# Optimization experiments

Hardware: AMD Instinct MI355X
Metric: run time of the kernel (lower is better)

## Reference

```python
import jax, jax.numpy as jnp
import numpy as np

B, S, D, H = 1, 2048, 1280, 16
HD = D // H  # 80


def setup_inputs() -> dict:
    key = jax.random.key(0)
    ks = jax.random.split(key, 6)
    return {
        "hidden_states": jax.random.normal(ks[0], (B, S, D), dtype=jnp.float32),
        "rotary_pos_emb": jax.random.normal(ks[1], (S, HD // 2), dtype=jnp.float32),
        "qkv_w": jax.random.normal(ks[2], (3 * D, D), dtype=jnp.float32) * 0.02,
        "qkv_b": jax.random.normal(ks[3], (3 * D,), dtype=jnp.float32) * 0.02,
        "proj_w": jax.random.normal(ks[4], (D, D), dtype=jnp.float32) * 0.02,
        "proj_b": jax.random.normal(ks[5], (D,), dtype=jnp.float32) * 0.02,
    }


def reference(hidden_states, rotary_pos_emb, qkv_w, qkv_b, proj_w, proj_b):
    b, s, d = hidden_states.shape
    h = H
    hd = d // h
    scaling = hd ** -0.5

    # fused QKV projection: [b, s, 3*d]
    qkv = hidden_states @ qkv_w.T + qkv_b
    qkv = qkv.reshape(b, s, 3, h, hd)
    q, k, v = qkv[:, :, 0], qkv[:, :, 1], qkv[:, :, 2]  # each [b, s, h, hd]

    # rotary embedding: cos/sin [s, hd//2] -> [1, s, 1, hd]
    cos = jnp.cos(rotary_pos_emb)
    sin = jnp.sin(rotary_pos_emb)
    cos = jnp.concatenate([cos, cos], axis=-1)[None, :, None, :]
    sin = jnp.concatenate([sin, sin], axis=-1)[None, :, None, :]

    def apply_rope(x):
        x1, x2 = x[..., : hd // 2], x[..., hd // 2:]
        return x * cos + jnp.concatenate([-x2, x1], axis=-1) * sin

    q = apply_rope(q)
    k = apply_rope(k)

    # [b, h, s, hd]
    q = q.transpose(0, 2, 1, 3)
    k = k.transpose(0, 2, 1, 3)
    v = v.transpose(0, 2, 1, 3)

    # naive full attention matrix [b, h, s, s]
    attn = jnp.einsum("bhqd,bhkd->bhqk", q, k) * scaling
    attn = jax.nn.softmax(attn, axis=-1)
    out = jnp.einsum("bhqk,bhkd->bhqd", attn, v)
    out = out.transpose(0, 2, 1, 3).reshape(b, s, d)
    return out @ proj_w.T + proj_b
```

## Files before the change

kernel.cpp:

```cpp
#include <hip/hip_runtime.h>
#include <math.h>

#define SS 2048
#define DD 1280
#define HH 16
#define HDD 80
#define ND3 3840
#define ZZ 2

typedef __attribute__((ext_vector_type(8))) short short8;
typedef __attribute__((ext_vector_type(4))) short s16x4;
typedef __attribute__((ext_vector_type(4))) float f32x4;
typedef __attribute__((ext_vector_type(8))) _Float16 h16x8;
typedef __attribute__((ext_vector_type(4))) _Float16 h16x4;

__device__ inline short f2bf(float f) {
    union { float f; unsigned u; } x; x.f = f;
    unsigned r = x.u + 0x7FFF + ((x.u >> 16) & 1);
    return (short)(r >> 16);
}

__device__ inline void gload_lds16(const void* g, void* l) {
    __builtin_amdgcn_global_load_lds(
        (const __attribute__((address_space(1))) void*)g,
        (__attribute__((address_space(3))) void*)l, 16, 0, 0);
}

__global__ __launch_bounds__(256) void split_f16(
    const float* __restrict__ a, _Float16* __restrict__ ah, int nbA,
    const float* __restrict__ b, _Float16* __restrict__ bh, int nbB,
    const float* __restrict__ c, _Float16* __restrict__ ch)
{
    const float* x; _Float16* h;
    int blk = blockIdx.x;
    if (blk < nbA)            { x = a; h = ah; }
    else if (blk < nbA + nbB) { blk -= nbA; x = b; h = bh; }
    else                      { blk -= nbA + nbB; x = c; h = ch; }
    int i = (blk * 256 + threadIdx.x) * 4;
    float4 v = *(const float4*)(x + i);
    h16x4 hv;
    hv[0] = (_Float16)v.x; hv[1] = (_Float16)v.y;
    hv[2] = (_Float16)v.z; hv[3] = (_Float16)v.w;
    *(h16x4*)(h + i) = hv;
}

#define LDSA(m, kg) ((m) * 32 + (((kg) ^ (((m) >> 1) & 3)) << 3))

template <int BMT, int BNT>
__global__ __launch_bounds__(256) void gemm_f16(
    const _Float16* __restrict__ Ah, const _Float16* __restrict__ Bh,
    const float* __restrict__ bias, float* __restrict__ C,
    int M, int N, int K)
{
    constexpr int IT = BMT / 32;
    constexpr int JT = BNT / 32;
    constexpr int AU = BMT / 64;
    constexpr int BU = BNT / 64;
    __shared__ _Float16 AhS[BMT * 32];
    __shared__ _Float16 BhS[BNT * 32];

    const int tid = threadIdx.x;
    const int w = tid >> 6;
    const int lane = tid & 63;
    const int l15 = lane & 15;
    const int quad = lane >> 4;
    const int wm = w >> 1, wn = w & 1;
    const int bm = blockIdx.y * BMT;
    const int bn = blockIdx.x * BNT;

    f32x4 acc[IT][JT];
    #pragma unroll
    for (int i = 0; i < IT; ++i)
        #pragma unroll
        for (int j = 0; j < JT; ++j)
            acc[i][j] = (f32x4){0.f, 0.f, 0.f, 0.f};

    for (int k0 = 0; k0 < K; k0 += 32) {
        __syncthreads();
        #pragma unroll
        for (int u = 0; u < AU; ++u) {
            int i = tid + u * 256;
            int m = i >> 2;
            int kg = (i & 3) ^ ((m >> 1) & 3);
            gload_lds16(Ah + (size_t)(bm + m) * K + k0 + kg * 8,
                        &AhS[(i & ~63) * 8]);
        }
        #pragma unroll
        for (int u = 0; u < BU; ++u) {
            int i = tid + u * 256;
            int m = i >> 2;
            int kg = (i & 3) ^ ((m >> 1) & 3);
            gload_lds16(Bh + (size_t)(bn + m) * K + k0 + kg * 8,
                        &BhS[(i & ~63) * 8]);
        }
        __syncthreads();

        h16x8 af[IT], bf[JT];
        #pragma unroll
        for (int i = 0; i < IT; ++i) {
            int m = wm * (BMT / 2) + i * 16 + l15;
            af[i] = *(h16x8*)&AhS[LDSA(m, quad)];
        }
        #pragma unroll
        for (int j = 0; j < JT; ++j) {
            int n = wn * (BNT / 2) + j * 16 + l15;
            bf[j] = *(h16x8*)&BhS[LDSA(n, quad)];
        }
        #pragma unroll
        for (int i = 0; i < IT; ++i)
            #pragma unroll
            for (int j = 0; j < JT; ++j)
                acc[i][j] = __builtin_amdgcn_mfma_f32_16x16x32_f16(af[i], bf[j], acc[i][j], 0, 0, 0);
    }

    #pragma unroll
    for (int j = 0; j < JT; ++j) {
        int col = bn + wn * (BNT / 2) + j * 16 + l15;
        float bb = bias[col];
        #pragma unroll
        for (int i = 0; i < IT; ++i)
            #pragma unroll
            for (int r = 0; r < 4; ++r) {
                int row = bm + wm * (BMT / 2) + i * 16 + quad * 4 + r;
                C[(size_t)row * N + col] = acc[i][j][r] + bb;
            }
    }
}

__global__ __launch_bounds__(256) void gemm_proj_merge(
    const _Float16* __restrict__ o_part, const float* __restrict__ l_part,
    const _Float16* __restrict__ Bh,
    const float* __restrict__ bias, float* __restrict__ C,
    int M, int N, int K)
{
    constexpr int BMT = 64, BNT = 128;
    constexpr int JT = BNT / 32;
    constexpr int BU = BNT / 64;
    __shared__ _Float16 AhS[BMT * 32];
    __shared__ _Float16 BhS[BNT * 32];
    __shared__ float linvS[HH * 64];

    const int tid = threadIdx.x;
    const int w = tid >> 6;
    const int lane = tid & 63;
    const int l15 = lane & 15;
    const int quad = lane >> 4;
    const int wm = w >> 1, wn = w & 1;
    const int bm = blockIdx.y * BMT;
    const int bn = blockIdx.x * BNT;

    for (int i = tid; i < HH * 64; i += 256) {
        int h = i >> 6, r = i & 63;
        float ls = 0.f;
        #pragma unroll
        for (int zi = 0; zi < ZZ; ++zi)
            ls += l_part[((size_t)zi * HH + h) * SS + bm + r];
        linvS[i] = 1.f / ls;
    }

    f32x4 acc[2][JT];
    #pragma unroll
    for (int i = 0; i < 2; ++i)
        #pragma unroll
        for (int j = 0; j < JT; ++j)
            acc[i][j] = (f32x4){0.f, 0.f, 0.f, 0.f};

    h16x8 ra[ZZ];
    auto loadgA = [&](int k0) {
        int m = tid >> 2, kg = tid & 3;
        size_t off = (size_t)(bm + m) * K + k0 + kg * 8;
        #pragma unroll
        for (int zi = 0; zi < ZZ; ++zi)
            ra[zi] = *(const h16x8*)(o_part + (size_t)zi * SS * DD + off);
    };

    loadgA(0);
    for (int k0 = 0; k0 < K; k0 += 32) {
        __syncthreads();
        {
            int m = tid >> 2, kg = tid & 3;
            int koff = k0 + kg * 8;
            int h = koff / HDD;
            float inv = linvS[h * 64 + m];
            h16x8 f;
            #pragma unroll
            for (int e = 0; e < 8; ++e) {
                float s = (float)ra[0][e];
                #pragma unroll
                for (int zi = 1; zi < ZZ; ++zi) s += (float)ra[zi][e];
                f[e] = (_Float16)(s * inv);
            }
            *(h16x8*)&AhS[LDSA(m, kg)] = f;
        }
        #pragma unroll
        for (int u = 0; u < BU; ++u) {
            int i = tid + u * 256;
            int m = i >> 2;
            int kg = (i & 3) ^ ((m >> 1) & 3);
            gload_lds16(Bh + (size_t)(bn + m) * K + k0 + kg * 8,
                        &BhS[(i & ~63) * 8]);
        }
        __syncthreads();
        if (k0 + 32 < K) loadgA(k0 + 32);

        h16x8 af[2], bf[JT];
        #pragma unroll
        for (int i = 0; i < 2; ++i) {
            int m = wm * 32 + i * 16 + l15;
            af[i] = *(h16x8*)&AhS[LDSA(m, quad)];
        }
        #pragma unroll
        for (int j = 0; j < JT; ++j) {
            int n = wn * 64 + j * 16 + l15;
            bf[j] = *(h16x8*)&BhS[LDSA(n, quad)];
        }
        #pragma unroll
        for (int i = 0; i < 2; ++i)
            #pragma unroll
            for (int j = 0; j < JT; ++j)
                acc[i][j] = __builtin_amdgcn_mfma_f32_16x16x32_f16(af[i], bf[j], acc[i][j], 0, 0, 0);
    }

    #pragma unroll
    for (int j = 0; j < JT; ++j) {
        int col = bn + wn * 64 + j * 16 + l15;
        float bb = bias[col];
        #pragma unroll
        for (int i = 0; i < 2; ++i)
            #pragma unroll
            for (int r = 0; r < 4; ++r) {
                int row = bm + wm * 32 + i * 16 + quad * 4 + r;
                C[(size_t)row * N + col] = acc[i][j][r] + bb;
            }
    }
}

__global__ __launch_bounds__(256) void rope_scatter_bf16(
    const float* __restrict__ qkv, const float* __restrict__ rpe,
    short* __restrict__ q, short* __restrict__ k, short* __restrict__ v)
{
    __shared__ __align__(16) float cs[40], sn[40];
    const int s = blockIdx.x;
    if (threadIdx.x < 40)
        __sincosf(rpe[s * 40 + threadIdx.x], &sn[threadIdx.x], &cs[threadIdx.x]);
    __syncthreads();
    const float scale = 0.11180339887498949f;
    const float* src = qkv + (size_t)s * ND3;
    for (int t = threadIdx.x; t < ND3 / 4; t += 256) {
        int j4 = t * 4;
        int p = j4 / DD;
        int rem = j4 - p * DD;
        int hh = rem / HDD;
        int d = rem - hh * HDD;
        float4 x = *(const float4*)(src + j4);
        float vv[4];
        if (p == 2) {
            vv[0] = x.x; vv[1] = x.y; vv[2] = x.z; vv[3] = x.w;
        } else {
            bool lo = d < 40;
            int dm = lo ? d : d - 40;
            float4 oth = *(const float4*)(src + p * DD + hh * HDD + (lo ? d + 40 : d - 40));
            float4 c4 = *(const float4*)&cs[dm];
            float4 s4 = *(const float4*)&sn[dm];
            float sg = lo ? -1.f : 1.f;
            vv[0] = x.x * c4.x + sg * oth.x * s4.x;
            vv[1] = x.y * c4.y + sg * oth.y * s4.y;
            vv[2] = x.z * c4.z + sg * oth.z * s4.z;
            vv[3] = x.w * c4.w + sg * oth.w * s4.w;
            if (p == 0) { vv[0] *= scale; vv[1] *= scale; vv[2] *= scale; vv[3] *= scale; }
        }
        short* dst = (p == 0) ? q : (p == 1) ? k : v;
        s16x4 o4;
        o4[0] = f2bf(vv[0]); o4[1] = f2bf(vv[1]);
        o4[2] = f2bf(vv[2]); o4[3] = f2bf(vv[3]);
        *(s16x4*)(dst + ((size_t)hh * SS + s) * HDD + d) = o4;
    }
}

__global__ __launch_bounds__(512, 4) void attn_mfma(
    const short* __restrict__ q, const short* __restrict__ k,
    const short* __restrict__ v, _Float16* __restrict__ o_part,
    float* __restrict__ l_part)
{
    __shared__ short Ks[64][104];
    __shared__ short Vts[80 * 64];
    __shared__ short Ps[8][16 * 64];

    const int h = blockIdx.y;
    const int q0 = blockIdx.x << 7;
    const int z = blockIdx.z;
    const int tid = threadIdx.x;
    const int w = tid >> 6;
    const int lane = tid & 63;
    const int l15 = lane & 15;
    const int quad = lane >> 4;

    const short* qbase = q + (size_t)h * SS * HDD;
    const short* kbase = k + (size_t)h * SS * HDD;
    const short* vbase = v + (size_t)h * SS * HDD;

    short8 qf[3];
    {
        const int row = q0 + w * 16 + l15;
        #pragma unroll
        for (int kk = 0; kk < 3; ++kk) {
            int c0 = kk * 32 + quad * 8;
            qf[kk] = (c0 < HDD) ? *(const short8*)(qbase + (size_t)row * HDD + c0)
                                : (short8)0;
        }
    }

    if (tid < 128) {
        int r = tid >> 1, c = 80 + (tid & 1) * 8;
        *(short8*)&Ks[r][c] = (short8)0;
    }

    float lsum[4] = {0.f, 0.f, 0.f, 0.f};
    f32x4 o[5];
    #pragma unroll
    for (int n = 0; n < 5; ++n) o[n] = (f32x4){0.f, 0.f, 0.f, 0.f};

    const int kt0 = z << 10;
    for (int kt = kt0; kt < kt0 + 1024; kt += 64) {
        __syncthreads();
        #pragma unroll
        for (int u = 0; u < 2; ++u) {
            int i = tid + u * 512;
            if (i < 640) {
                int r = i / 10, c = (i - r * 10) * 8;
                *(short8*)&Ks[r][c] = *(const short8*)(kbase + (size_t)(kt + r) * HDD + c);
            }
        }
        {
            int task = tid;
            if (task < 320) {
                int r4 = (task & 15) << 2;
                int d4 = (task >> 4) << 2;
                s16x4 a0 = *(const s16x4*)(vbase + (size_t)(kt + r4 + 0) * HDD + d4);
                s16x4 a1 = *(const s16x4*)(vbase + (size_t)(kt + r4 + 1) * HDD + d4);
                s16x4 a2 = *(const s16x4*)(vbase + (size_t)(kt + r4 + 2) * HDD + d4);
                s16x4 a3 = *(const s16x4*)(vbase + (size_t)(kt + r4 + 3) * HDD + d4);
                #pragma unroll
                for (int j = 0; j < 4; ++j) {
                    s16x4 w4 = {a0[j], a1[j], a2[j], a3[j]};
                    int d = d4 + j;
                    int sw = (r4 >> 3) ^ (d & 7);
                    *(s16x4*)&Vts[d * 64 + sw * 8 + (r4 & 7)] = w4;
                }
            }
        }
        __syncthreads();

        f32x4 s_[4];
        #pragma unroll
        for (int nt = 0; nt < 4; ++nt) {
            short8 bf0 = *(short8*)&Ks[nt * 16 + l15][quad * 8];
            short8 bf1 = *(short8*)&Ks[nt * 16 + l15][32 + quad * 8];
            short8 bf2 = *(short8*)&Ks[nt * 16 + l15][64 + quad * 8];
            f32x4 acc = (f32x4){0.f, 0.f, 0.f, 0.f};
            acc = __builtin_amdgcn_mfma_f32_16x16x32_bf16(qf[0], bf0, acc, 0, 0, 0);
            acc = __builtin_amdgcn_mfma_f32_16x16x32_bf16(qf[1], bf1, acc, 0, 0, 0);
            acc = __builtin_amdgcn_mfma_f32_16x16x32_bf16(qf[2], bf2, acc, 0, 0, 0);
            s_[nt] = acc;
        }

        #pragma unroll
        for (int nt = 0; nt < 4; ++nt)
            #pragma unroll
            for (int r = 0; r < 4; ++r) {
                float p = __expf(s_[nt][r] - 8.f);
                lsum[r] += p;
                int row = quad * 4 + r;
                int g = (nt * 2 + (l15 >> 3)) ^ (row & 7);
                Ps[w][row * 64 + g * 8 + (l15 & 7)] = f2bf(p);
            }

        short8 pf[2];
        #pragma unroll
        for (int kk = 0; kk < 2; ++kk) {
            int g = (kk * 4 + quad) ^ (l15 & 7);
            pf[kk] = *(short8*)&Ps[w][l15 * 64 + g * 8];
        }
        #pragma unroll
        for (int n = 0; n < 5; ++n) {
            #pragma unroll
            for (int kk = 0; kk < 2; ++kk) {
                int d = n * 16 + l15;
                int sw = (kk * 4 + quad) ^ (l15 & 7);
                short8 vf = *(short8*)&Vts[d * 64 + sw * 8];
                o[n] = __builtin_amdgcn_mfma_f32_16x16x32_bf16(pf[kk], vf, o[n], 0, 0, 0);
            }
        }
    }

    _Float16* ob = o_part + (size_t)z * SS * DD;
    #pragma unroll
    for (int r = 0; r < 4; ++r) {
        float rs = lsum[r];
        #pragma unroll
        for (int off = 1; off < 16; off <<= 1)
            rs += __shfl_xor(rs, off, 64);
        lsum[r] = rs;
    }
    #pragma unroll
    for (int n = 0; n < 5; ++n)
        #pragma unroll
        for (int r = 0; r < 4; ++r) {
            int row = q0 + w * 16 + quad * 4 + r;
            ob[(size_t)row * DD + h * HDD + n * 16 + l15] = (_Float16)o[n][r];
        }
    if (l15 == 0)
        #pragma unroll
        for (int r = 0; r < 4; ++r)
            l_part[((size_t)z * HH + h) * SS + q0 + w * 16 + quad * 4 + r] = lsum[r];
}

extern "C" void kernel_launch(void* const* d_in, const int* in_sizes, int n_in,
                              void* d_out, int out_size, void* d_ws, size_t ws_size,
                              hipStream_t stream)
{
    const float* hs     = (const float*)d_in[0];
    const float* rpe    = (const float*)d_in[1];
    const float* qkv_w  = (const float*)d_in[2];
    const float* qkv_b  = (const float*)d_in[3];
    const float* proj_w = (const float*)d_in[4];
    const float* proj_b = (const float*)d_in[5];
    float* out = (float*)d_out;

    short* s0 = (short*)d_ws;
    float* qkv_f  = (float*)d_ws;
    _Float16* o_part = (_Float16*)s0;
    float* l_part = (float*)(s0 + 10485760);
    short* s1 = s0 + 15728640;
    _Float16* qkvw_h = (_Float16*)s1;
    short* qb = s1;
    short* kb = s1 + 2621440;
    short* vb = s1 + 5242880;
    short* s2 = s1 + 7864320;
    _Float16* hs_h = (_Float16*)s2;
    short* s3 = s2 + 2621440;
    _Float16* projw_h = (_Float16*)s3;

    const int n_hs = SS * DD;
    const int n_qw = ND3 * DD;
    const int n_pw = DD * DD;

    split_f16<<<n_hs / 1024 + n_qw / 1024 + n_pw / 1024, 256, 0, stream>>>(
        hs, hs_h, n_hs / 1024,
        qkv_w, qkvw_h, n_qw / 1024,
        proj_w, projw_h);
    gemm_f16<128, 128><<<dim3(ND3 / 128, SS / 128), 256, 0, stream>>>(
        hs_h, qkvw_h, qkv_b, qkv_f, SS, ND3, DD);
    rope_scatter_bf16<<<SS, 256, 0, stream>>>(qkv_f, rpe, qb, kb, vb);
    attn_mfma<<<dim3(SS / 128, HH, ZZ), 512, 0, stream>>>(qb, kb, vb, o_part, l_part);
    gemm_proj_merge<<<dim3(DD / 128, SS / 64), 256, 0, stream>>>(
        o_part, l_part, projw_h, proj_b, out, SS, DD, DD);
}
```

Before: 213.8 us.

## Double-buffer LDS tiles in QKV and projection GEMMs to overlap loads with MFMA

Both the generic f16 GEMM and the projection-merge GEMM now keep two LDS buffers for their weight tiles (and for A in the generic GEMM). The next K-slice is issued with global_load_lds before the current slice's MFMAs run, so load latency can overlap compute and one barrier per iteration is removed. The cost is double the LDS footprint, which may reduce occupancy. Correctness relies on the async LDS loads having completed by the trailing barrier, since no explicit vmcnt wait is added.

```diff
diff --git a/kernel.cpp b/kernel.cpp
--- a/kernel.cpp
+++ b/kernel.cpp
@@ -56,8 +56,8 @@
     constexpr int JT = BNT / 32;
     constexpr int AU = BMT / 64;
     constexpr int BU = BNT / 64;
-    __shared__ _Float16 AhS[BMT * 32];
-    __shared__ _Float16 BhS[BNT * 32];
+    __shared__ _Float16 AhS[2][BMT * 32];
+    __shared__ _Float16 BhS[2][BNT * 32];
 
     const int tid = threadIdx.x;
     const int w = tid >> 6;
@@ -75,15 +75,14 @@
         for (int j = 0; j < JT; ++j)
             acc[i][j] = (f32x4){0.f, 0.f, 0.f, 0.f};
 
-    for (int k0 = 0; k0 < K; k0 += 32) {
-        __syncthreads();
+    auto stage = [&](int buf, int k0) {
         #pragma unroll
         for (int u = 0; u < AU; ++u) {
             int i = tid + u * 256;
             int m = i >> 2;
             int kg = (i & 3) ^ ((m >> 1) & 3);
             gload_lds16(Ah + (size_t)(bm + m) * K + k0 + kg * 8,
-                        &AhS[(i & ~63) * 8]);
+                        &AhS[buf][(i & ~63) * 8]);
         }
         #pragma unroll
         for (int u = 0; u < BU; ++u) {
@@ -91,26 +90,35 @@
             int m = i >> 2;
             int kg = (i & 3) ^ ((m >> 1) & 3);
             gload_lds16(Bh + (size_t)(bn + m) * K + k0 + kg * 8,
-                        &BhS[(i & ~63) * 8]);
-        }
-        __syncthreads();
+                        &BhS[buf][(i & ~63) * 8]);
+        }
+    };
+
+    stage(0, 0);
+    __syncthreads();
+    int cur = 0;
+    for (int k0 = 0; k0 < K; k0 += 32) {
+        if (k0 + 32 < K) stage(cur ^ 1, k0 + 32);
 
         h16x8 af[IT], bf[JT];
         #pragma unroll
         for (int i = 0; i < IT; ++i) {
             int m = wm * (BMT / 2) + i * 16 + l15;
-            af[i] = *(h16x8*)&AhS[LDSA(m, quad)];
+            af[i] = *(h16x8*)&AhS[cur][LDSA(m, quad)];
         }
         #pragma unroll
         for (int j = 0; j < JT; ++j) {
             int n = wn * (BNT / 2) + j * 16 + l15;
-            bf[j] = *(h16x8*)&BhS[LDSA(n, quad)];
+            bf[j] = *(h16x8*)&BhS[cur][LDSA(n, quad)];
         }
         #pragma unroll
         for (int i = 0; i < IT; ++i)
             #pragma unroll
             for (int j = 0; j < JT; ++j)
                 acc[i][j] = __builtin_amdgcn_mfma_f32_16x16x32_f16(af[i], bf[j], acc[i][j], 0, 0, 0);
+
+        __syncthreads();
+        cur ^= 1;
     }
 
     #pragma unroll
@@ -137,7 +145,7 @@
     constexpr int JT = BNT / 32;
     constexpr int BU = BNT / 64;
     __shared__ _Float16 AhS[BMT * 32];
-    __shared__ _Float16 BhS[BNT * 32];
+    __shared__ _Float16 BhS[2][BNT * 32];
     __shared__ float linvS[HH * 64];
 
     const int tid = threadIdx.x;
@@ -173,10 +181,22 @@
         for (int zi = 0; zi < ZZ; ++zi)
             ra[zi] = *(const h16x8*)(o_part + (size_t)zi * SS * DD + off);
     };
-
+    auto stageB = [&](int buf, int k0) {
+        #pragma unroll
+        for (int u = 0; u < BU; ++u) {
+            int i = tid + u * 256;
+            int m = i >> 2;
+            int kg = (i & 3) ^ ((m >> 1) & 3);
+            gload_lds16(Bh + (size_t)(bn + m) * K + k0 + kg * 8,
+                        &BhS[buf][(i & ~63) * 8]);
+        }
+    };
+
+    stageB(0, 0);
     loadgA(0);
+    __syncthreads();
+    int cur = 0;
     for (int k0 = 0; k0 < K; k0 += 32) {
-        __syncthreads();
         {
             int m = tid >> 2, kg = tid & 3;
             int koff = k0 + kg * 8;
@@ -192,16 +212,12 @@
             }
             *(h16x8*)&AhS[LDSA(m, kg)] = f;
         }
-        #pragma unroll
-        for (int u = 0; u < BU; ++u) {
-            int i = tid + u * 256;
-            int m = i >> 2;
-            int kg = (i & 3) ^ ((m >> 1) & 3);
-            gload_lds16(Bh + (size_t)(bn + m) * K + k0 + kg * 8,
-                        &BhS[(i & ~63) * 8]);
-        }
         __syncthreads();
-        if (k0 + 32 < K) loadgA(k0 + 32);
+
+        if (k0 + 32 < K) {
+            stageB(cur ^ 1, k0 + 32);
+            loadgA(k0 + 32);
+        }
 
         h16x8 af[2], bf[JT];
         #pragma unroll
@@ -212,13 +228,16 @@
         #pragma unroll
         for (int j = 0; j < JT; ++j) {
             int n = wn * 64 + j * 16 + l15;
-            bf[j] = *(h16x8*)&BhS[LDSA(n, quad)];
+            bf[j] = *(h16x8*)&BhS[cur][LDSA(n, quad)];
         }
         #pragma unroll
         for (int i = 0; i < 2; ++i)
             #pragma unroll
             for (int j = 0; j < JT; ++j)
                 acc[i][j] = __builtin_amdgcn_mfma_f32_16x16x32_f16(af[i], bf[j], acc[i][j], 0, 0, 0);
+
+        __syncthreads();
+        cur ^= 1;
     }
 
     #pragma unroll
```

Measured after the change: 211.2 us. No clear change (-1.2%).
